# Optimization experiments

Hardware: AMD Instinct MI355X
Metric: run time of the kernel (lower is better)

## Reference

```python
import jax, jax.numpy as jnp
import numpy as np

N_CTX = 4096
D_MODEL = 2048


def setup_inputs() -> dict:
    key = jax.random.key(0)
    k1, k2, k3 = jax.random.split(key, 3)
    embedding = jax.random.normal(k1, (N_CTX, D_MODEL), dtype=jnp.float32)
    # torch.rand -> uniform [0, 1)
    qk = jax.random.uniform(k2, (D_MODEL, D_MODEL), dtype=jnp.float32)
    ov = jax.random.uniform(k3, (D_MODEL, D_MODEL), dtype=jnp.float32)
    return {"embedding": embedding, "qk": qk, "ov": ov}


def reference(embedding, qk, ov):
    n = embedding.shape[0]
    # scores[i, j] = e_i @ qk @ e_j  -> [N, N]
    scores = (embedding @ qk) @ embedding.T
    # strict upper triangle gets -inf (causal mask), matching triu(-inf, diag=1)
    causal_mask = jnp.triu(jnp.full((n, n), -jnp.inf, dtype=scores.dtype), k=1)
    scores = scores + causal_mask
    attn = jax.nn.softmax(scores, axis=-1)  # nn.Softmax() on 2D -> dim=1
    return (attn @ embedding) @ ov
```

## Files before the change

### kernel.cpp

```cpp
#include <hip/hip_runtime.h>
#include <hip/hip_bf16.h>

#define N_CTX 4096
#define DM    2048

typedef __attribute__((ext_vector_type(8))) short short8;
typedef __attribute__((ext_vector_type(4))) float f32x4;
typedef unsigned short ushort_t;

__device__ __forceinline__ ushort_t f2bf(float x) {
    __hip_bfloat16 h = __float2bfloat16(x);
    return __builtin_bit_cast(ushort_t, h);
}
__device__ __forceinline__ float bf2f(ushort_t u) {
    return __bfloat162float(__builtin_bit_cast(__hip_bfloat16, u));
}

__device__ __forceinline__ void gload16(const void* g, void* l) {
    __builtin_amdgcn_global_load_lds((const __attribute__((address_space(1))) void*)g,
                                     (__attribute__((address_space(3))) void*)l,
                                     16, 0, 0);
}


__global__ __launch_bounds__(256) void split_cast_kernel(
    const float* __restrict__ in, ushort_t* __restrict__ hi, ushort_t* __restrict__ lo, int n4)
{
    int idx = blockIdx.x * 256 + threadIdx.x;
    if (idx >= n4) return;
    float4 v = reinterpret_cast<const float4*>(in)[idx];
    float vv[4] = {v.x, v.y, v.z, v.w};
    ushort_t h[4], l[4];
#pragma unroll
    for (int j = 0; j < 4; ++j) {
        h[j] = f2bf(vv[j]);
        l[j] = f2bf(vv[j] - bf2f(h[j]));
    }
    reinterpret_cast<ushort4*>(hi)[idx] = *reinterpret_cast<ushort4*>(h);
    reinterpret_cast<ushort4*>(lo)[idx] = *reinterpret_cast<ushort4*>(l);
}

template <bool SPLIT>
__global__ __launch_bounds__(256) void transpose_cast_kernel(
    const float* __restrict__ in, ushort_t* __restrict__ hi, ushort_t* __restrict__ lo,
    int R, int C)
{
    __shared__ float tile[32][33];
    int bc = blockIdx.x * 32;
    int br = blockIdx.y * 32;
    int tx = threadIdx.x, ty = threadIdx.y;
#pragma unroll
    for (int r = ty; r < 32; r += 8)
        tile[r][tx] = in[(size_t)(br + r) * C + bc + tx];
    __syncthreads();
#pragma unroll
    for (int c = ty; c < 32; c += 8) {
        float v = tile[tx][c];
        size_t o = (size_t)(bc + c) * R + br + tx;
        ushort_t h = f2bf(v);
        hi[o] = h;
        if (SPLIT) lo[o] = f2bf(v - bf2f(h));
    }
}


template <int OM, bool CAUSAL>
__global__ __launch_bounds__(256, 2) void gemm_split_kernel(
    const ushort_t* __restrict__ Ah, const ushort_t* __restrict__ Al,
    const ushort_t* __restrict__ Bh, const ushort_t* __restrict__ Bl,
    int K, int ldc,
    float* __restrict__ Cf, ushort_t* __restrict__ Ch, ushort_t* __restrict__ Cl)
{
    const int bx = blockIdx.x;
    const int by = blockIdx.y;
    if (CAUSAL && bx * 128 > by * 128 + 127) return;

    __shared__ ushort_t AHs[128 * 64];
    __shared__ ushort_t ALs[128 * 64];
    __shared__ ushort_t BHs[128 * 64];
    __shared__ ushort_t BLs[128 * 64];

    const int t = threadIdx.x;
    const int l = t & 63;
    const int w = t >> 6;
    const int wr = w >> 1;
    const int wc = w & 1;

    f32x4 acc[4][4];
#pragma unroll
    for (int m = 0; m < 4; ++m)
#pragma unroll
        for (int n = 0; n < 4; ++n) acc[m][n] = (f32x4){0.f, 0.f, 0.f, 0.f};

    const size_t arow0 = (size_t)by * 128;
    const size_t brow0 = (size_t)bx * 128;

    auto stage1 = [&](const ushort_t* src, ushort_t* dst, size_t row0, int kt) {
#pragma unroll
        for (int i = 0; i < 4; ++i) {
            int f = i * 256 + t;
            int r = f >> 3;
            int cch = (f & 7) ^ (r & 7);
            gload16(src + (row0 + r) * (size_t)K + kt + cch * 8,
                    (char*)dst + (i * 256 + w * 64) * 16);
        }
    };
    auto rdf = [&](short8* d, const ushort_t* base, int rbase, int kk) {
#pragma unroll
        for (int m = 0; m < 4; ++m) {
            int row = rbase + m * 16 + (l & 15);
            int gby = kk * 64 + (l >> 4) * 16;
            d[m] = *(const short8*)((const char*)base + row * 128 +
                                    (gby ^ ((row & 7) * 16)));
        }
    };
    auto mm16 = [&](const short8* a, const short8* b) {
#pragma unroll
        for (int m = 0; m < 4; ++m)
#pragma unroll
            for (int n = 0; n < 4; ++n)
                acc[m][n] = __builtin_amdgcn_mfma_f32_16x16x32_bf16(
                    a[m], b[n], acc[m][n], 0, 0, 0);
    };

    for (int kt = 0; kt < K; kt += 64) {
        __syncthreads();
        stage1(Ah, AHs, arow0, kt);
        stage1(Al, ALs, arow0, kt);
        stage1(Bh, BHs, brow0, kt);
        stage1(Bl, BLs, brow0, kt);
        __syncthreads();

#pragma unroll
        for (int kk = 0; kk < 2; ++kk) {
            short8 ah[4], bh[4], x[4];
            rdf(ah, AHs, wr * 64, kk);
            rdf(bh, BHs, wc * 64, kk);
            mm16(ah, bh);
            rdf(x, BLs, wc * 64, kk);
            mm16(ah, x);
            rdf(x, ALs, wr * 64, kk);
            mm16(x, bh);
        }
    }

    const int r0 = by * 128 + wr * 64 + ((l >> 4) << 2);
    const int c0 = bx * 128 + wc * 64 + (l & 15);
#pragma unroll
    for (int m = 0; m < 4; ++m)
#pragma unroll
        for (int n = 0; n < 4; ++n)
#pragma unroll
            for (int j = 0; j < 4; ++j) {
                size_t o = (size_t)(r0 + m * 16 + j) * ldc + (c0 + n * 16);
                float v = acc[m][n][j];
                if (OM == 0) {
                    Cf[o] = v;
                } else {
                    ushort_t hh = f2bf(v);
                    Ch[o] = hh;
                    Cl[o] = f2bf(v - bf2f(hh));
                }
            }
}


template <int OM, bool CKLIM>
__global__ __launch_bounds__(256, 2) void gemm_bt_kernel(
    const ushort_t* __restrict__ A, const ushort_t* __restrict__ B,
    int K, int ldc,
    float* __restrict__ Cf, ushort_t* __restrict__ Ch)
{
    const int bx = blockIdx.x;
    const int by = blockIdx.y;

    __shared__ ushort_t Asm[128 * 64];
    __shared__ ushort_t Bsm[128 * 64];

    const int t = threadIdx.x;
    const int l = t & 63;
    const int w = t >> 6;
    const int wr = w >> 1;
    const int wc = w & 1;

    f32x4 acc[4][4];
#pragma unroll
    for (int m = 0; m < 4; ++m)
#pragma unroll
        for (int n = 0; n < 4; ++n) acc[m][n] = (f32x4){0.f, 0.f, 0.f, 0.f};

    const size_t arow0 = (size_t)by * 128;
    const size_t brow0 = (size_t)bx * 128;

    int kend = K;
    if (CKLIM) { int lim = (by + 1) * 128; if (lim < kend) kend = lim; }

    for (int kt = 0; kt < kend; kt += 64) {
        __syncthreads();
#pragma unroll
        for (int i = 0; i < 4; ++i) {
            int f = i * 256 + t;
            int r = f >> 3;
            int cch = (f & 7) ^ (r & 7);
            gload16(A + (arow0 + r) * (size_t)K + kt + cch * 8,
                    (char*)Asm + (i * 256 + w * 64) * 16);
            gload16(B + (brow0 + r) * (size_t)K + kt + cch * 8,
                    (char*)Bsm + (i * 256 + w * 64) * 16);
        }
        __syncthreads();

#pragma unroll
        for (int kk = 0; kk < 2; ++kk) {
            short8 af[4], bfr[4];
#pragma unroll
            for (int m = 0; m < 4; ++m) {
                int row = wr * 64 + m * 16 + (l & 15);
                int gby = kk * 64 + (l >> 4) * 16;
                af[m] = *(const short8*)((const char*)Asm + row * 128 +
                                         (gby ^ ((row & 7) * 16)));
            }
#pragma unroll
            for (int n = 0; n < 4; ++n) {
                int row = wc * 64 + n * 16 + (l & 15);
                int gby = kk * 64 + (l >> 4) * 16;
                bfr[n] = *(const short8*)((const char*)Bsm + row * 128 +
                                          (gby ^ ((row & 7) * 16)));
            }
#pragma unroll
            for (int m = 0; m < 4; ++m)
#pragma unroll
                for (int n = 0; n < 4; ++n)
                    acc[m][n] = __builtin_amdgcn_mfma_f32_16x16x32_bf16(
                        af[m], bfr[n], acc[m][n], 0, 0, 0);
        }
    }

    const int r0 = by * 128 + wr * 64 + ((l >> 4) << 2);
    const int c0 = bx * 128 + wc * 64 + (l & 15);
#pragma unroll
    for (int m = 0; m < 4; ++m)
#pragma unroll
        for (int n = 0; n < 4; ++n)
#pragma unroll
            for (int j = 0; j < 4; ++j) {
                size_t o = (size_t)(r0 + m * 16 + j) * ldc + (c0 + n * 16);
                if (OM == 0) Cf[o] = acc[m][n][j];
                else         Ch[o] = f2bf(acc[m][n][j]);
            }
}


__device__ __forceinline__ float waveMax(float v) {
#pragma unroll
    for (int o = 32; o > 0; o >>= 1) v = fmaxf(v, __shfl_xor(v, o, 64));
    return v;
}
__device__ __forceinline__ float waveSum(float v) {
#pragma unroll
    for (int o = 32; o > 0; o >>= 1) v += __shfl_xor(v, o, 64);
    return v;
}

__global__ __launch_bounds__(256) void softmax_kernel(
    const float* __restrict__ S, ushort_t* __restrict__ A)
{
    const int i = blockIdx.x;
    __shared__ float row[N_CTX];
    __shared__ float red[8];
    const int t = threadIdx.x;
    const int len = i + 1;
    const float* Srow = S + (size_t)i * N_CTX;

    float m = -3.4e38f;
    for (int j = t; j < len; j += 256) {
        float v = Srow[j];
        row[j] = v;
        m = fmaxf(m, v);
    }
    m = waveMax(m);
    if ((t & 63) == 0) red[t >> 6] = m;
    __syncthreads();
    m = fmaxf(fmaxf(red[0], red[1]), fmaxf(red[2], red[3]));

    float s = 0.f;
    for (int j = t; j < len; j += 256) {
        float e = __expf(row[j] - m);
        row[j] = e;
        s += e;
    }
    s = waveSum(s);
    __syncthreads();
    if ((t & 63) == 0) red[t >> 6] = s;
    __syncthreads();
    float inv = 1.f / (red[0] + red[1] + red[2] + red[3]);

    ushort_t* Arow = A + (size_t)i * N_CTX;
    for (int j = t; j < N_CTX; j += 256)
        Arow[j] = (j < len) ? f2bf(row[j] * inv) : (ushort_t)0;
}


extern "C" void kernel_launch(void* const* d_in, const int* in_sizes, int n_in,
                              void* d_out, int out_size, void* d_ws, size_t ws_size,
                              hipStream_t stream)
{
    const float* E  = (const float*)d_in[0];
    const float* qk = (const float*)d_in[1];
    const float* ov = (const float*)d_in[2];
    float* out = (float*)d_out;

    char* ws = (char*)d_ws;
    size_t off = 0;
    auto take = [&](size_t bytes) -> char* {
        char* p = ws + off;
        off += (bytes + 255) & ~(size_t)255;
        return p;
    };

    ushort_t* Ehi   = (ushort_t*)take((size_t)N_CTX * DM * 2);
    ushort_t* Elo   = (ushort_t*)take((size_t)N_CTX * DM * 2);
    ushort_t* Et    = (ushort_t*)take((size_t)N_CTX * DM * 2);
    ushort_t* QKthi = (ushort_t*)take((size_t)DM * DM * 2);
    ushort_t* QKtlo = (ushort_t*)take((size_t)DM * DM * 2);
    ushort_t* OVt   = (ushort_t*)take((size_t)DM * DM * 2);
    ushort_t* Qhi   = (ushort_t*)take((size_t)N_CTX * DM * 2);
    ushort_t* Qlo   = (ushort_t*)take((size_t)N_CTX * DM * 2);
    float*    S     = (float*)take((size_t)N_CTX * N_CTX * 4);
    ushort_t* Attn  = (ushort_t*)take((size_t)N_CTX * N_CTX * 2);
    ushort_t* Hbf   = (ushort_t*)take((size_t)N_CTX * DM * 2);
    (void)ws_size; (void)in_sizes; (void)n_in; (void)out_size;

    split_cast_kernel<<<dim3((N_CTX * DM / 4) / 256), 256, 0, stream>>>(E, Ehi, Elo, N_CTX * DM / 4);
    transpose_cast_kernel<true ><<<dim3(DM / 32, DM / 32),    dim3(32, 8), 0, stream>>>(qk, QKthi, QKtlo, DM, DM);
    transpose_cast_kernel<false><<<dim3(DM / 32, DM / 32),    dim3(32, 8), 0, stream>>>(ov, OVt, nullptr, DM, DM);
    transpose_cast_kernel<false><<<dim3(DM / 32, N_CTX / 32), dim3(32, 8), 0, stream>>>(E, Et, nullptr, N_CTX, DM);

    gemm_split_kernel<2, false><<<dim3(DM / 128, N_CTX / 128), 256, 0, stream>>>(
        Ehi, Elo, QKthi, QKtlo, DM, DM, nullptr, Qhi, Qlo);

    gemm_split_kernel<0, true><<<dim3(N_CTX / 128, N_CTX / 128), 256, 0, stream>>>(
        Qhi, Qlo, Ehi, Elo, DM, N_CTX, S, nullptr, nullptr);

    softmax_kernel<<<N_CTX, 256, 0, stream>>>(S, Attn);

    gemm_bt_kernel<1, true><<<dim3(DM / 128, N_CTX / 128), 256, 0, stream>>>(
        Attn, Et, N_CTX, DM, nullptr, Hbf);

    gemm_bt_kernel<0, false><<<dim3(DM / 128, N_CTX / 128), 256, 0, stream>>>(
        Hbf, OVt, DM, DM, out, nullptr);
}
```

Measured before the change: 469.0 us.

## Double-buffer LDS in GEMM kernels and launch only lower-triangular score tiles

Both GEMM kernels now use two LDS buffers, so the global-to-LDS loads for the next k-tile are issued before computing on the current one, and there is one barrier per iteration instead of two. The split GEMM halves its k-tile to 32 so the doubled buffers keep the same LDS footprint, and it uses a new swizzle. The causal score GEMM launches a 1D grid covering only the lower-triangular tiles and maps each block index to a row and column with a sqrt. This removes the empty blocks that used to exit early. The cost is more LDS in gemm_bt, which now uses 64KB and may lower occupancy, plus more loop iterations in the split kernel.

```diff
diff --git a/kernel.cpp b/kernel.cpp
--- a/kernel.cpp
+++ b/kernel.cpp
@@ -1,5 +1,6 @@
 #include <hip/hip_runtime.h>
 #include <hip/hip_bf16.h>
+#include <math.h>
 
 #define N_CTX 4096
 #define DM    2048
@@ -64,27 +65,33 @@
 }
 
 
-template <int OM, bool CAUSAL>
+template <int OM, bool TRI>
 __global__ __launch_bounds__(256, 2) void gemm_split_kernel(
     const ushort_t* __restrict__ Ah, const ushort_t* __restrict__ Al,
     const ushort_t* __restrict__ Bh, const ushort_t* __restrict__ Bl,
     int K, int ldc,
     float* __restrict__ Cf, ushort_t* __restrict__ Ch, ushort_t* __restrict__ Cl)
 {
-    const int bx = blockIdx.x;
-    const int by = blockIdx.y;
-    if (CAUSAL && bx * 128 > by * 128 + 127) return;
-
-    __shared__ ushort_t AHs[128 * 64];
-    __shared__ ushort_t ALs[128 * 64];
-    __shared__ ushort_t BHs[128 * 64];
-    __shared__ ushort_t BLs[128 * 64];
+    int bx, by;
+    if (TRI) {
+        int i = blockIdx.x;
+        int b = (int)((sqrtf(8.f * (float)i + 1.f) - 1.f) * 0.5f);
+        while ((b + 1) * (b + 2) / 2 <= i) ++b;
+        while (b * (b + 1) / 2 > i) --b;
+        by = b; bx = i - b * (b + 1) / 2;
+    } else {
+        bx = blockIdx.x; by = blockIdx.y;
+    }
+
+    __shared__ ushort_t lds[2][4][128 * 32];
 
     const int t = threadIdx.x;
     const int l = t & 63;
     const int w = t >> 6;
     const int wr = w >> 1;
     const int wc = w & 1;
+    const int lr = l & 15;
+    const int lc = l >> 4;
 
     f32x4 acc[4][4];
 #pragma unroll
@@ -95,23 +102,27 @@
     const size_t arow0 = (size_t)by * 128;
     const size_t brow0 = (size_t)bx * 128;
 
-    auto stage1 = [&](const ushort_t* src, ushort_t* dst, size_t row0, int kt) {
-#pragma unroll
-        for (int i = 0; i < 4; ++i) {
-            int f = i * 256 + t;
-            int r = f >> 3;
-            int cch = (f & 7) ^ (r & 7);
-            gload16(src + (row0 + r) * (size_t)K + kt + cch * 8,
-                    (char*)dst + (i * 256 + w * 64) * 16);
+    auto stg1 = [&](const ushort_t* src, ushort_t* dst, size_t row0, int kt) {
+#pragma unroll
+        for (int i2 = 0; i2 < 2; ++i2) {
+            int f = i2 * 256 + t;
+            int r = f >> 2, c = f & 3;
+            gload16(src + (row0 + r) * (size_t)K + kt + ((c ^ ((r >> 1) & 3)) << 3),
+                    (char*)dst + f * 16);
         }
     };
-    auto rdf = [&](short8* d, const ushort_t* base, int rbase, int kk) {
+    auto stage = [&](int kt, int buf) {
+        stg1(Ah, lds[buf][0], arow0, kt);
+        stg1(Al, lds[buf][1], arow0, kt);
+        stg1(Bh, lds[buf][2], brow0, kt);
+        stg1(Bl, lds[buf][3], brow0, kt);
+    };
+    auto rdf = [&](short8* d, const ushort_t* base, int rbase) {
 #pragma unroll
         for (int m = 0; m < 4; ++m) {
-            int row = rbase + m * 16 + (l & 15);
-            int gby = kk * 64 + (l >> 4) * 16;
-            d[m] = *(const short8*)((const char*)base + row * 128 +
-                                    (gby ^ ((row & 7) * 16)));
+            int row = rbase + m * 16 + lr;
+            d[m] = *(const short8*)((const char*)base + row * 64 +
+                                    ((lc ^ ((row >> 1) & 3)) << 4));
         }
     };
     auto mm16 = [&](const short8* a, const short8* b) {
@@ -123,29 +134,25 @@
                     a[m], b[n], acc[m][n], 0, 0, 0);
     };
 
-    for (int kt = 0; kt < K; kt += 64) {
+    stage(0, 0);
+    __syncthreads();
+    const int nt = K >> 5;
+    for (int tt = 0; tt < nt; ++tt) {
+        const int buf = tt & 1;
+        if (tt + 1 < nt) stage((tt + 1) << 5, buf ^ 1);
+        short8 ah[4], bh[4], x[4];
+        rdf(ah, lds[buf][0], wr * 64);
+        rdf(bh, lds[buf][2], wc * 64);
+        mm16(ah, bh);
+        rdf(x, lds[buf][3], wc * 64);
+        mm16(ah, x);
+        rdf(x, lds[buf][1], wr * 64);
+        mm16(x, bh);
         __syncthreads();
-        stage1(Ah, AHs, arow0, kt);
-        stage1(Al, ALs, arow0, kt);
-        stage1(Bh, BHs, brow0, kt);
-        stage1(Bl, BLs, brow0, kt);
-        __syncthreads();
-
-#pragma unroll
-        for (int kk = 0; kk < 2; ++kk) {
-            short8 ah[4], bh[4], x[4];
-            rdf(ah, AHs, wr * 64, kk);
-            rdf(bh, BHs, wc * 64, kk);
-            mm16(ah, bh);
-            rdf(x, BLs, wc * 64, kk);
-            mm16(ah, x);
-            rdf(x, ALs, wr * 64, kk);
-            mm16(x, bh);
-        }
-    }
-
-    const int r0 = by * 128 + wr * 64 + ((l >> 4) << 2);
-    const int c0 = bx * 128 + wc * 64 + (l & 15);
+    }
+
+    const int r0 = by * 128 + wr * 64 + (lc << 2);
+    const int c0 = bx * 128 + wc * 64 + lr;
 #pragma unroll
     for (int m = 0; m < 4; ++m)
 #pragma unroll
@@ -174,8 +181,7 @@
     const int bx = blockIdx.x;
     const int by = blockIdx.y;
 
-    __shared__ ushort_t Asm[128 * 64];
-    __shared__ ushort_t Bsm[128 * 64];
+    __shared__ ushort_t lds[2][2][128 * 64];
 
     const int t = threadIdx.x;
     const int l = t & 63;
@@ -195,20 +201,24 @@
     int kend = K;
     if (CKLIM) { int lim = (by + 1) * 128; if (lim < kend) kend = lim; }
 
-    for (int kt = 0; kt < kend; kt += 64) {
-        __syncthreads();
-#pragma unroll
-        for (int i = 0; i < 4; ++i) {
-            int f = i * 256 + t;
-            int r = f >> 3;
-            int cch = (f & 7) ^ (r & 7);
-            gload16(A + (arow0 + r) * (size_t)K + kt + cch * 8,
-                    (char*)Asm + (i * 256 + w * 64) * 16);
-            gload16(B + (brow0 + r) * (size_t)K + kt + cch * 8,
-                    (char*)Bsm + (i * 256 + w * 64) * 16);
+    auto stage = [&](int kt, int buf) {
+#pragma unroll
+        for (int i2 = 0; i2 < 4; ++i2) {
+            int f = i2 * 256 + t;
+            int r = f >> 3, c = f & 7;
+            gload16(A + (arow0 + r) * (size_t)K + kt + ((c ^ (r & 7)) << 3),
+                    (char*)lds[buf][0] + f * 16);
+            gload16(B + (brow0 + r) * (size_t)K + kt + ((c ^ (r & 7)) << 3),
+                    (char*)lds[buf][1] + f * 16);
         }
-        __syncthreads();
-
+    };
+
+    stage(0, 0);
+    __syncthreads();
+    const int nt = kend >> 6;
+    for (int tt = 0; tt < nt; ++tt) {
+        const int buf = tt & 1;
+        if (tt + 1 < nt) stage((tt + 1) << 6, buf ^ 1);
 #pragma unroll
         for (int kk = 0; kk < 2; ++kk) {
             short8 af[4], bfr[4];
@@ -216,14 +226,14 @@
             for (int m = 0; m < 4; ++m) {
                 int row = wr * 64 + m * 16 + (l & 15);
                 int gby = kk * 64 + (l >> 4) * 16;
-                af[m] = *(const short8*)((const char*)Asm + row * 128 +
+                af[m] = *(const short8*)((const char*)lds[buf][0] + row * 128 +
                                          (gby ^ ((row & 7) * 16)));
             }
 #pragma unroll
             for (int n = 0; n < 4; ++n) {
                 int row = wc * 64 + n * 16 + (l & 15);
                 int gby = kk * 64 + (l >> 4) * 16;
-                bfr[n] = *(const short8*)((const char*)Bsm + row * 128 +
+                bfr[n] = *(const short8*)((const char*)lds[buf][1] + row * 128 +
                                           (gby ^ ((row & 7) * 16)));
             }
 #pragma unroll
@@ -233,6 +243,7 @@
                     acc[m][n] = __builtin_amdgcn_mfma_f32_16x16x32_bf16(
                         af[m], bfr[n], acc[m][n], 0, 0, 0);
         }
+        __syncthreads();
     }
 
     const int r0 = by * 128 + wr * 64 + ((l >> 4) << 2);
@@ -338,7 +349,7 @@
     gemm_split_kernel<2, false><<<dim3(DM / 128, N_CTX / 128), 256, 0, stream>>>(
         Ehi, Elo, QKthi, QKtlo, DM, DM, nullptr, Qhi, Qlo);
 
-    gemm_split_kernel<0, true><<<dim3(N_CTX / 128, N_CTX / 128), 256, 0, stream>>>(
+    gemm_split_kernel<0, true><<<dim3(32 * 33 / 2), 256, 0, stream>>>(
         Qhi, Qlo, Ehi, Elo, DM, N_CTX, S, nullptr, nullptr);
 
     softmax_kernel<<<N_CTX, 256, 0, stream>>>(S, Attn);
```

Result: no change. 460.1 us (-1.9%).
